# Kernel tuning notes

Measured on AMD Instinct MI355X. Metric: run time of the kernel, lower is better.

Reference implementation:

```python
import jax, jax.numpy as jnp
import numpy as np

T = 2048
HIDDEN = 4096
H = 32
HKV = 8
D = 128
THETA = 10000.0


def setup_inputs() -> dict:
    key = jax.random.key(0)
    k1, k2, k3, k4, k5 = jax.random.split(key, 5)
    s = 0.02
    return {
        "x": jax.random.normal(k1, (T, 2 * HIDDEN), dtype=jnp.float32),
        "positions": jnp.arange(T, dtype=jnp.int32),
        "Wq": jax.random.normal(k2, (H * D, 2 * HIDDEN), dtype=jnp.float32) * s,
        "Wk": jax.random.normal(k3, (HKV * D, 2 * HIDDEN), dtype=jnp.float32) * s,
        "Wv": jax.random.normal(k4, (HKV * D, 2 * HIDDEN), dtype=jnp.float32) * s,
        "Wo": jax.random.normal(k5, (HIDDEN, H * D), dtype=jnp.float32) * s,
    }


def _rope_cos_sin(positions):
    # NeoX-style: cos_sin_cache[pos] = [cos(freqs), sin(freqs)], freqs over head_dim/2
    inv_freq = 1.0 / (THETA ** (jnp.arange(0, D, 2, dtype=jnp.float32) / D))
    freqs = positions.astype(jnp.float32)[:, None] * inv_freq  # [T, D/2]
    return jnp.cos(freqs)[:, None, :], jnp.sin(freqs)[:, None, :]  # broadcast over heads


def _apply_rope(t, cos, sin):
    half = D // 2
    t1, t2 = t[..., :half], t[..., half:]
    return jnp.concatenate([t1 * cos - t2 * sin, t2 * cos + t1 * sin], axis=-1)


def reference(x, positions, Wq, Wk, Wv, Wo):
    n = x.shape[0]
    q = (x @ Wq.T).reshape(n, H, D)
    k = (x @ Wk.T).reshape(n, HKV, D)
    v = (x @ Wv.T).reshape(n, HKV, D)
    cos, sin = _rope_cos_sin(positions)
    q = _apply_rope(q, cos, sin)
    k = _apply_rope(k, cos, sin)
    # cache starts empty -> k_full/v_full are just k/v; prefill (n>1) -> causal
    G = H // HKV  # GQA group size; avoid materializing repeated K/V
    qg = q.reshape(n, HKV, G, D)
    scale = D ** -0.5
    scores = jnp.einsum("tkgd,skd->kgts", qg, k) * scale  # [HKV, G, T, T]
    causal = jnp.arange(n)[:, None] >= jnp.arange(n)[None, :]
    scores = jnp.where(causal, scores, jnp.finfo(scores.dtype).min)
    p = jax.nn.softmax(scores, axis=-1)
    o = jnp.einsum("kgts,skd->tkgd", p, v).reshape(n, H * D)
    return o @ Wo.T
```

## Files before the change

### kernel.cpp

```cpp
#include <hip/hip_runtime.h>
#include <hip/hip_bf16.h>
#include <math.h>

typedef unsigned short u16;
typedef u16 u16x8 __attribute__((ext_vector_type(8)));
typedef __bf16 bf16x8 __attribute__((ext_vector_type(8)));
typedef float f32x4 __attribute__((ext_vector_type(4)));

#define T_SEQ 2048
#define IN_DIM 8192
#define QKV_COLS 6144
#define O_COLS 4096

__device__ __forceinline__ u16 f2bf(float f){
  unsigned u = __builtin_bit_cast(unsigned, f);
  u += 0x7fffu + ((u >> 16) & 1u);
  return (u16)(u >> 16);
}
__device__ __forceinline__ float bf2f(u16 h){
  unsigned u = ((unsigned)h) << 16;
  return __builtin_bit_cast(float, u);
}
__device__ __forceinline__ void gload16(const void* g, void* l){
  __builtin_amdgcn_global_load_lds((const __attribute__((address_space(1))) unsigned*)g,
                                   (__attribute__((address_space(3))) unsigned*)l, 16, 0, 0);
}
__device__ __forceinline__ void storeC(float* p, float v){ *p = v; }
__device__ __forceinline__ void storeC(u16* p, float v){ *p = f2bf(v); }

__global__ void cvt_all(const float* __restrict__ x, const float* __restrict__ wq,
                        const float* __restrict__ wk, const float* __restrict__ wv,
                        const float* __restrict__ wo,
                        u16* __restrict__ xb, u16* __restrict__ wb, u16* __restrict__ wob){
  const int NX  = T_SEQ*IN_DIM/4;
  const int NQ  = 4096*IN_DIM/4;
  const int NKV = 1024*IN_DIM/4;
  const int NO  = 4096*4096/4;
  const int TOT = NX + NQ + 2*NKV + NO;
  int stride = gridDim.x * blockDim.x;
  for (int i = blockIdx.x*blockDim.x + threadIdx.x; i < TOT; i += stride){
    const float4* s; ushort4* d; int j = i;
    if (j < NX){ s = (const float4*)x; d = (ushort4*)xb; }
    else { j -= NX;
      if (j < NQ){ s = (const float4*)wq; d = (ushort4*)wb; }
      else { j -= NQ;
        if (j < NKV){ s = (const float4*)wk; d = (ushort4*)(wb + (size_t)4096*IN_DIM); }
        else { j -= NKV;
          if (j < NKV){ s = (const float4*)wv; d = (ushort4*)(wb + (size_t)5120*IN_DIM); }
          else { j -= NKV; s = (const float4*)wo; d = (ushort4*)wob; } } } }
    float4 v = s[j];
    ushort4 o; o.x = f2bf(v.x); o.y = f2bf(v.y); o.z = f2bf(v.z); o.w = f2bf(v.w);
    d[j] = o;
  }
}

__global__ void rope_scale_kernel(u16* __restrict__ qkv, const int* __restrict__ pos){
  __shared__ float cs[64], sn[64];
  int t = blockIdx.x;
  int p = pos[t];
  if (threadIdx.x < 64){
    int i = threadIdx.x;
    double e = (double)(2*i) / 128.0;
    float invf = (float)pow(10000.0, -e);
    float ang = (float)p * invf;
    cs[i] = cosf(ang);
    sn[i] = sinf(ang);
  }
  __syncthreads();
  u16* row = qkv + (size_t)t * QKV_COLS;
  const float qscale = 0.08838834764831845f;
  for (int idx = threadIdx.x; idx < 40*64; idx += blockDim.x){
    int head = idx >> 6, i = idx & 63;
    int base = (head < 32) ? head*128 : 4096 + (head-32)*128;
    float sc = (head < 32) ? qscale : 1.0f;
    float t1 = bf2f(row[base + i]);
    float t2 = bf2f(row[base + i + 64]);
    row[base + i]      = f2bf((t1*cs[i] - t2*sn[i]) * sc);
    row[base + i + 64] = f2bf((t2*cs[i] + t1*sn[i]) * sc);
  }
}

template<typename OutT, int NFRAG>
__global__ __launch_bounds__(512,2) void gemm_pipe(const u16* __restrict__ A, const u16* __restrict__ B,
                                                   OutT* __restrict__ C, int K, int ldc, int ntile_n){
  __shared__ __attribute__((aligned(16))) u16 Asm[4*8192];
  __shared__ __attribute__((aligned(16))) u16 Bsm[4*NFRAG*2048];
  const int tid = threadIdx.x;
  const int w = tid >> 6, l = tid & 63;
  const int wm = w >> 2, wn = w & 3;
  const int lr = l & 15, lg = l >> 4;
  const int id = blockIdx.x;
  const int m0 = (id & 7) * 256;
  const int n0 = (id >> 3) * (NFRAG*64);
  const int BBUF = NFRAG*4096;

  const int srow  = tid >> 2;
  const int sslot = ((tid & 3) - ((tid >> 3) & 3)) & 3;
  const u16* Ag  = A + (size_t)(m0 + srow) * K + sslot * 8;
  const u16* Bg  = B + (size_t)(n0 + srow) * K + sslot * 8;
  const u16* Bg2 = B + (size_t)(n0 + 128 + srow) * K + sslot * 8;
  char* AsB = (char*)Asm;
  char* BsB = (char*)Bsm;
  const int sdst = w * 1024;

  int aoff[8], boff[NFRAG];
  #pragma unroll
  for (int i = 0; i < 8; ++i){
    int ra = wm*128 + i*16 + lr;
    aoff[i] = ra*64 + (((lg + (ra>>1)) & 3) << 4);
  }
  #pragma unroll
  for (int i = 0; i < NFRAG; ++i){
    int rb = wn*(NFRAG*16) + i*16 + lr;
    boff[i] = rb*64 + (((lg + (rb>>1)) & 3) << 4);
  }

  f32x4 acc[8][NFRAG];
  #pragma unroll
  for (int m = 0; m < 8; ++m)
    #pragma unroll
    for (int n = 0; n < NFRAG; ++n)
      acc[m][n] = (f32x4){0.f,0.f,0.f,0.f};

  const int NT = K >> 5;

  #define STAGE_TILE(tt) do { \
    const int nb_ = ((tt) & 3); \
    gload16(Ag + (tt)*32,                 AsB + nb_*16384 +        sdst); \
    gload16(Ag + (size_t)128*K + (tt)*32, AsB + nb_*16384 + 8192 + sdst); \
    gload16(Bg + (tt)*32,                 BsB + nb_*BBUF +         sdst); \
    if (NFRAG == 3 && tid < 256) \
      gload16(Bg2 + (tt)*32,              BsB + nb_*BBUF + 8192 +  sdst); \
  } while(0)

  STAGE_TILE(0);
  STAGE_TILE(1);

  for (int t = 0; t < NT; ++t){
    const int ab = (t & 3) * 16384;
    const int bb = (t & 3) * BBUF;
    if (t == NT-1){
      asm volatile("s_waitcnt vmcnt(0)" ::: "memory");
    } else if (NFRAG == 3){
      if (w < 4) asm volatile("s_waitcnt vmcnt(4)" ::: "memory");
      else       asm volatile("s_waitcnt vmcnt(3)" ::: "memory");
    } else {
      asm volatile("s_waitcnt vmcnt(3)" ::: "memory");
    }
    __builtin_amdgcn_s_barrier();
    __builtin_amdgcn_sched_barrier(0);

    bf16x8 bfr[NFRAG], afr[8];
    #pragma unroll
    for (int n = 0; n < NFRAG; ++n) bfr[n] = *(const bf16x8*)(BsB + bb + boff[n]);
    #pragma unroll
    for (int i = 0; i < 8; ++i)     afr[i] = *(const bf16x8*)(AsB + ab + aoff[i]);

    if (t + 2 < NT) STAGE_TILE(t+2);

    __builtin_amdgcn_s_setprio(1);
    #pragma unroll
    for (int i = 0; i < 8; ++i)
      #pragma unroll
      for (int n = 0; n < NFRAG; ++n)
        acc[i][n] = __builtin_amdgcn_mfma_f32_16x16x32_bf16(afr[i], bfr[n], acc[i][n], 0, 0, 0);
    __builtin_amdgcn_s_setprio(0);
  }
  #undef STAGE_TILE

  #pragma unroll
  for (int m = 0; m < 8; ++m)
    #pragma unroll
    for (int n = 0; n < NFRAG; ++n)
      #pragma unroll
      for (int r = 0; r < 4; ++r){
        int row = m0 + wm*128 + m*16 + lg*4 + r;
        int col = n0 + wn*(NFRAG*16) + n*16 + lr;
        storeC(&C[(size_t)row*ldc + col], acc[m][n][r]);
      }
}

__global__ __launch_bounds__(256) void attn_kernel(const u16* __restrict__ qkv, u16* __restrict__ ob){
  __shared__ __attribute__((aligned(16))) u16 Ksm[32*128];
  __shared__ __attribute__((aligned(16))) u16 Vt[128*40];
  __shared__ __attribute__((aligned(16))) u16 Psm[4][32*40];
  const int tid = threadIdx.x, l = tid & 63, w = tid >> 6;
  const int lr = l & 15, lg = l >> 4;
  const int qb = (gridDim.x - 1) - blockIdx.x;
  const int kv = blockIdx.y;
  const int h = kv*4 + w;
  const int q0 = qb * 32;

  bf16x8 aq[2][4];
  #pragma unroll
  for (int mm = 0; mm < 2; ++mm)
    #pragma unroll
    for (int kk = 0; kk < 4; ++kk)
      aq[mm][kk] = *(const bf16x8*)(qkv + (size_t)(q0 + mm*16 + lr)*QKV_COLS + h*128 + kk*32 + lg*8);

  f32x4 oacc[2][8] = {};
  float mrun[2][4], lrun[2][4];
  #pragma unroll
  for (int mm=0;mm<2;mm++)
    #pragma unroll
    for (int r=0;r<4;r++){ mrun[mm][r] = -1e30f; lrun[mm][r] = 0.f; }

  const int cbv = ((tid & 15) << 4) | (tid >> 4);
  for (int kt = 0; kt <= qb; ++kt){
    const int s0 = kt * 32;
    #pragma unroll
    for (int i = 0; i < 2; ++i){
      int c = tid + i*256, s = c >> 4, dq = c & 15;
      u16x8 kvv = *(const u16x8*)(qkv + (size_t)(s0+s)*QKV_COLS + 4096 + kv*128 + dq*8);
      int lin = (s << 8) + (dq << 4); lin ^= (s & 7) << 4;
      *(u16x8*)((char*)Ksm + lin) = kvv;
    }
    #pragma unroll
    for (int i = 0; i < 2; ++i){
      int c = cbv + i*256, s = c >> 4, dq = c & 15;
      u16x8 vv = *(const u16x8*)(qkv + (size_t)(s0+s)*QKV_COLS + 5120 + kv*128 + dq*8);
      #pragma unroll
      for (int j = 0; j < 8; ++j) Vt[(dq*8+j)*40 + s] = vv[j];
    }
    __syncthreads();

    f32x4 sa[2][2] = {};
    #pragma unroll
    for (int kk = 0; kk < 4; ++kk){
      bf16x8 bk[2];
      #pragma unroll
      for (int nn = 0; nn < 2; ++nn){
        int srow = nn*16 + lr;
        int lin = (srow << 8) + (kk << 6) + (lg << 4); lin ^= (srow & 7) << 4;
        bk[nn] = *(const bf16x8*)((char*)Ksm + lin);
      }
      #pragma unroll
      for (int mm = 0; mm < 2; ++mm)
        #pragma unroll
        for (int nn = 0; nn < 2; ++nn)
          sa[mm][nn] = __builtin_amdgcn_mfma_f32_16x16x32_bf16(aq[mm][kk], bk[nn], sa[mm][nn], 0,0,0);
    }

    if (kt == qb){
      #pragma unroll
      for (int mm=0;mm<2;mm++)
        #pragma unroll
        for (int nn=0;nn<2;nn++)
          #pragma unroll
          for (int r=0;r<4;r++){
            int qrel = mm*16 + lg*4 + r, srel = nn*16 + lr;
            if (srel > qrel) sa[mm][nn][r] = -1e30f;
          }
    }

    float alph[2][4];
    #pragma unroll
    for (int mm=0;mm<2;mm++)
      #pragma unroll
      for (int r=0;r<4;r++){
        float v = fmaxf(sa[mm][0][r], sa[mm][1][r]);
        v = fmaxf(v, __shfl_xor(v, 1));
        v = fmaxf(v, __shfl_xor(v, 2));
        v = fmaxf(v, __shfl_xor(v, 4));
        v = fmaxf(v, __shfl_xor(v, 8));
        float mn = fmaxf(mrun[mm][r], v);
        float al = __expf(mrun[mm][r] - mn);
        float p0 = __expf(sa[mm][0][r] - mn);
        float p1 = __expf(sa[mm][1][r] - mn);
        sa[mm][0][r] = p0; sa[mm][1][r] = p1;
        float rs = p0 + p1;
        rs += __shfl_xor(rs, 1);
        rs += __shfl_xor(rs, 2);
        rs += __shfl_xor(rs, 4);
        rs += __shfl_xor(rs, 8);
        lrun[mm][r] = lrun[mm][r]*al + rs;
        mrun[mm][r] = mn;
        alph[mm][r] = al;
      }
    #pragma unroll
    for (int mm=0;mm<2;mm++)
      #pragma unroll
      for (int df=0;df<8;df++)
        #pragma unroll
        for (int r=0;r<4;r++)
          oacc[mm][df][r] *= alph[mm][r];

    #pragma unroll
    for (int mm=0;mm<2;mm++)
      #pragma unroll
      for (int nn=0;nn<2;nn++)
        #pragma unroll
        for (int r=0;r<4;r++)
          Psm[w][(mm*16 + lg*4 + r)*40 + nn*16 + lr] = f2bf(sa[mm][nn][r]);

    bf16x8 ap[2];
    #pragma unroll
    for (int mm=0;mm<2;mm++)
      ap[mm] = *(const bf16x8*)(&Psm[w][(mm*16 + lr)*40 + lg*8]);
    #pragma unroll
    for (int df=0;df<8;df++){
      bf16x8 bv = *(const bf16x8*)(&Vt[(df*16 + lr)*40 + lg*8]);
      #pragma unroll
      for (int mm=0;mm<2;mm++)
        oacc[mm][df] = __builtin_amdgcn_mfma_f32_16x16x32_bf16(ap[mm], bv, oacc[mm][df], 0,0,0);
    }
    __syncthreads();
  }

  #pragma unroll
  for (int mm=0;mm<2;mm++)
    #pragma unroll
    for (int df=0;df<8;df++)
      #pragma unroll
      for (int r=0;r<4;r++){
        float val = oacc[mm][df][r] / lrun[mm][r];
        int t = q0 + mm*16 + lg*4 + r;
        int col = h*128 + df*16 + lr;
        ob[(size_t)t*O_COLS + col] = f2bf(val);
      }
}

extern "C" void kernel_launch(void* const* d_in, const int* in_sizes, int n_in,
                              void* d_out, int out_size, void* d_ws, size_t ws_size,
                              hipStream_t stream){
  const float* x  = (const float*)d_in[0];
  const int*   pos= (const int*)d_in[1];
  const float* Wq = (const float*)d_in[2];
  const float* Wk = (const float*)d_in[3];
  const float* Wv = (const float*)d_in[4];
  const float* Wo = (const float*)d_in[5];
  float* out = (float*)d_out;

  char* ws = (char*)d_ws;
  u16* xb   = (u16*)(ws);
  u16* wb   = (u16*)(ws + 33554432);
  u16* wob  = (u16*)(ws + 134217728);
  u16* qkv  = (u16*)(ws + 167772160);
  u16* obuf = (u16*)(ws + 192937984);

  cvt_all<<<2048, 256, 0, stream>>>(x, Wq, Wk, Wv, Wo, xb, wb, wob);

  gemm_pipe<u16,3><<<256, 512, 0, stream>>>(xb, wb, qkv, IN_DIM, QKV_COLS, 32);
  rope_scale_kernel<<<T_SEQ, 256, 0, stream>>>(qkv, pos);
  attn_kernel<<<dim3(64,8), 256, 0, stream>>>(qkv, obuf);
  gemm_pipe<float,2><<<256, 512, 0, stream>>>(obuf, wob, out, O_COLS, O_COLS, 32);
}
```

Measured before the change: 853.3 us.

## Pre-transpose V globally and double-buffer K/V via async LDS loads in attention

Adds a separate kernel that writes V transposed into a workspace buffer, so the attention kernel no longer does per-element scalar transposes into shared memory each tile. The attention kernel now uses 64-key tiles, issues direct global-to-LDS loads for K (double buffered) and V, and uses waitcnt plus barriers so the next tiles load while the current tile computes. It also raises occupancy hints and sets wave priority around the MFMA blocks. The cost is an extra kernel launch and an extra pass over V in global memory, plus more shared memory per block.

After: 782.5 us. 8.3% less time.

```diff
diff --git a/kernel.cpp b/kernel.cpp
--- a/kernel.cpp
+++ b/kernel.cpp
@@ -80,6 +80,29 @@
   }
 }
 
+__global__ void transpose_v(const u16* __restrict__ qkv, u16* __restrict__ vtg){
+  __shared__ u16 tl[128][72];
+  const int head = blockIdx.y;
+  const int st = blockIdx.x;
+  const int tid = threadIdx.x;
+  #pragma unroll
+  for (int i = 0; i < 4; ++i){
+    int c = tid + i*256, s = c >> 4, dq = c & 15;
+    u16x8 v = *(const u16x8*)(qkv + (size_t)(st*64+s)*QKV_COLS + 5120 + head*128 + dq*8);
+    #pragma unroll
+    for (int j = 0; j < 8; ++j) tl[dq*8+j][s] = v[j];
+  }
+  __syncthreads();
+  #pragma unroll
+  for (int i = 0; i < 4; ++i){
+    int c = tid + i*256, d = c >> 3, sq = c & 7;
+    u16x8 v;
+    #pragma unroll
+    for (int j = 0; j < 8; ++j) v[j] = tl[d][sq*8+j];
+    *(u16x8*)(vtg + (size_t)head*262144 + (size_t)d*2048 + st*64 + sq*8) = v;
+  }
+}
+
 template<typename OutT, int NFRAG>
 __global__ __launch_bounds__(512,2) void gemm_pipe(const u16* __restrict__ A, const u16* __restrict__ B,
                                                    OutT* __restrict__ C, int K, int ldc, int ntile_n){
@@ -180,16 +203,18 @@
       }
 }
 
-__global__ __launch_bounds__(256) void attn_kernel(const u16* __restrict__ qkv, u16* __restrict__ ob){
-  __shared__ __attribute__((aligned(16))) u16 Ksm[32*128];
-  __shared__ __attribute__((aligned(16))) u16 Vt[128*40];
-  __shared__ __attribute__((aligned(16))) u16 Psm[4][32*40];
+__global__ __launch_bounds__(256,2) void attn2(const u16* __restrict__ qkv, const u16* __restrict__ vtg,
+                                               u16* __restrict__ ob){
+  __shared__ __attribute__((aligned(16))) u16 Ksm[2*64*128];
+  __shared__ __attribute__((aligned(16))) u16 Vsm[128*64];
+  __shared__ __attribute__((aligned(16))) u16 Psm[4][32*72];
   const int tid = threadIdx.x, l = tid & 63, w = tid >> 6;
   const int lr = l & 15, lg = l >> 4;
-  const int qb = (gridDim.x - 1) - blockIdx.x;
+  const int qb = 63 - (int)blockIdx.x;
   const int kv = blockIdx.y;
   const int h = kv*4 + w;
   const int q0 = qb * 32;
+  const int lastkt = (qb*32 + 31) >> 6;
 
   bf16x8 aq[2][4];
   #pragma unroll
@@ -198,77 +223,92 @@
     for (int kk = 0; kk < 4; ++kk)
       aq[mm][kk] = *(const bf16x8*)(qkv + (size_t)(q0 + mm*16 + lr)*QKV_COLS + h*128 + kk*32 + lg*8);
 
+  const u16* Ksrc[4]; const u16* Vsrc[4];
+  #pragma unroll
+  for (int i = 0; i < 4; ++i){
+    int c = (i*4 + w)*64 + l;
+    int s = c >> 4, cp = c & 15;
+    Ksrc[i] = qkv + (size_t)s*QKV_COLS + 4096 + kv*128 + ((cp ^ (s & 7)) * 8);
+    int d = c >> 3, cp2 = c & 7;
+    Vsrc[i] = vtg + (size_t)kv*262144 + (size_t)d*2048 + ((cp2 ^ (d & 7)) * 8);
+  }
+  char* KsB = (char*)Ksm;
+  char* VsB = (char*)Vsm;
+
+  #define STAGE_K(kt) do { const int bo_ = ((kt)&1)*16384; \
+    _Pragma("unroll") for (int i_ = 0; i_ < 4; ++i_) \
+      gload16(Ksrc[i_] + (size_t)(kt)*64*QKV_COLS, KsB + bo_ + (i_*4+w)*1024); } while(0)
+  #define STAGE_V(kt) do { \
+    _Pragma("unroll") for (int i_ = 0; i_ < 4; ++i_) \
+      gload16(Vsrc[i_] + (kt)*64, VsB + (i_*4+w)*1024); } while(0)
+
+  STAGE_K(0);
+  STAGE_V(0);
+  if (lastkt >= 1) STAGE_K(1);
+
   f32x4 oacc[2][8] = {};
   float mrun[2][4], lrun[2][4];
   #pragma unroll
-  for (int mm=0;mm<2;mm++)
-    #pragma unroll
-    for (int r=0;r<4;r++){ mrun[mm][r] = -1e30f; lrun[mm][r] = 0.f; }
-
-  const int cbv = ((tid & 15) << 4) | (tid >> 4);
-  for (int kt = 0; kt <= qb; ++kt){
-    const int s0 = kt * 32;
-    #pragma unroll
-    for (int i = 0; i < 2; ++i){
-      int c = tid + i*256, s = c >> 4, dq = c & 15;
-      u16x8 kvv = *(const u16x8*)(qkv + (size_t)(s0+s)*QKV_COLS + 4096 + kv*128 + dq*8);
-      int lin = (s << 8) + (dq << 4); lin ^= (s & 7) << 4;
-      *(u16x8*)((char*)Ksm + lin) = kvv;
-    }
-    #pragma unroll
-    for (int i = 0; i < 2; ++i){
-      int c = cbv + i*256, s = c >> 4, dq = c & 15;
-      u16x8 vv = *(const u16x8*)(qkv + (size_t)(s0+s)*QKV_COLS + 5120 + kv*128 + dq*8);
-      #pragma unroll
-      for (int j = 0; j < 8; ++j) Vt[(dq*8+j)*40 + s] = vv[j];
-    }
-    __syncthreads();
-
-    f32x4 sa[2][2] = {};
+  for (int mm = 0; mm < 2; ++mm)
+    #pragma unroll
+    for (int r = 0; r < 4; ++r){ mrun[mm][r] = -1e30f; lrun[mm][r] = 0.f; }
+
+  for (int kt = 0; kt <= lastkt; ++kt){
+    if (kt < lastkt) asm volatile("s_waitcnt vmcnt(8)" ::: "memory");
+    else             asm volatile("s_waitcnt vmcnt(4)" ::: "memory");
+    __builtin_amdgcn_s_barrier();
+    const int kb = (kt & 1) * 16384;
+
+    f32x4 sa[2][4] = {};
+    __builtin_amdgcn_s_setprio(1);
     #pragma unroll
     for (int kk = 0; kk < 4; ++kk){
-      bf16x8 bk[2];
-      #pragma unroll
-      for (int nn = 0; nn < 2; ++nn){
-        int srow = nn*16 + lr;
-        int lin = (srow << 8) + (kk << 6) + (lg << 4); lin ^= (srow & 7) << 4;
-        bk[nn] = *(const bf16x8*)((char*)Ksm + lin);
+      bf16x8 bk[4];
+      #pragma unroll
+      for (int nn = 0; nn < 4; ++nn){
+        int row = nn*16 + lr;
+        bk[nn] = *(const bf16x8*)(KsB + kb + row*256 + (((kk*4 + lg) ^ (row & 7)) << 4));
       }
       #pragma unroll
       for (int mm = 0; mm < 2; ++mm)
         #pragma unroll
-        for (int nn = 0; nn < 2; ++nn)
+        for (int nn = 0; nn < 4; ++nn)
           sa[mm][nn] = __builtin_amdgcn_mfma_f32_16x16x32_bf16(aq[mm][kk], bk[nn], sa[mm][nn], 0,0,0);
     }
-
-    if (kt == qb){
-      #pragma unroll
-      for (int mm=0;mm<2;mm++)
-        #pragma unroll
-        for (int nn=0;nn<2;nn++)
+    __builtin_amdgcn_s_setprio(0);
+
+    if (kt == lastkt){
+      #pragma unroll
+      for (int mm = 0; mm < 2; ++mm)
+        #pragma unroll
+        for (int nn = 0; nn < 4; ++nn)
           #pragma unroll
-          for (int r=0;r<4;r++){
-            int qrel = mm*16 + lg*4 + r, srel = nn*16 + lr;
+          for (int r = 0; r < 4; ++r){
+            int srel = kt*64 + nn*16 + lr;
+            int qrel = q0 + mm*16 + lg*4 + r;
             if (srel > qrel) sa[mm][nn][r] = -1e30f;
           }
     }
 
     float alph[2][4];
     #pragma unroll
-    for (int mm=0;mm<2;mm++)
-      #pragma unroll
-      for (int r=0;r<4;r++){
-        float v = fmaxf(sa[mm][0][r], sa[mm][1][r]);
+    for (int mm = 0; mm < 2; ++mm)
+      #pragma unroll
+      for (int r = 0; r < 4; ++r){
+        float v = fmaxf(fmaxf(sa[mm][0][r], sa[mm][1][r]), fmaxf(sa[mm][2][r], sa[mm][3][r]));
         v = fmaxf(v, __shfl_xor(v, 1));
         v = fmaxf(v, __shfl_xor(v, 2));
         v = fmaxf(v, __shfl_xor(v, 4));
         v = fmaxf(v, __shfl_xor(v, 8));
         float mn = fmaxf(mrun[mm][r], v);
         float al = __expf(mrun[mm][r] - mn);
-        float p0 = __expf(sa[mm][0][r] - mn);
-        float p1 = __expf(sa[mm][1][r] - mn);
-        sa[mm][0][r] = p0; sa[mm][1][r] = p1;
-        float rs = p0 + p1;
+        float rs = 0.f;
+        #pragma unroll
+        for (int nn = 0; nn < 4; ++nn){
+          float p = __expf(sa[mm][nn][r] - mn);
+          sa[mm][nn][r] = p;
+          rs += p;
+        }
         rs += __shfl_xor(rs, 1);
         rs += __shfl_xor(rs, 2);
         rs += __shfl_xor(rs, 4);
@@ -278,41 +318,63 @@
         alph[mm][r] = al;
       }
     #pragma unroll
-    for (int mm=0;mm<2;mm++)
-      #pragma unroll
-      for (int df=0;df<8;df++)
-        #pragma unroll
-        for (int r=0;r<4;r++)
+    for (int mm = 0; mm < 2; ++mm)
+      #pragma unroll
+      for (int df = 0; df < 8; ++df)
+        #pragma unroll
+        for (int r = 0; r < 4; ++r)
           oacc[mm][df][r] *= alph[mm][r];
 
-    #pragma unroll
-    for (int mm=0;mm<2;mm++)
-      #pragma unroll
-      for (int nn=0;nn<2;nn++)
-        #pragma unroll
-        for (int r=0;r<4;r++)
-          Psm[w][(mm*16 + lg*4 + r)*40 + nn*16 + lr] = f2bf(sa[mm][nn][r]);
-
-    bf16x8 ap[2];
-    #pragma unroll
-    for (int mm=0;mm<2;mm++)
-      ap[mm] = *(const bf16x8*)(&Psm[w][(mm*16 + lr)*40 + lg*8]);
-    #pragma unroll
-    for (int df=0;df<8;df++){
-      bf16x8 bv = *(const bf16x8*)(&Vt[(df*16 + lr)*40 + lg*8]);
-      #pragma unroll
-      for (int mm=0;mm<2;mm++)
-        oacc[mm][df] = __builtin_amdgcn_mfma_f32_16x16x32_bf16(ap[mm], bv, oacc[mm][df], 0,0,0);
+    if (kt < lastkt) asm volatile("s_waitcnt vmcnt(4)" ::: "memory");
+    else             asm volatile("s_waitcnt vmcnt(0)" ::: "memory");
+    __builtin_amdgcn_s_barrier();
+
+    #pragma unroll
+    for (int mm = 0; mm < 2; ++mm)
+      #pragma unroll
+      for (int nn = 0; nn < 4; ++nn)
+        #pragma unroll
+        for (int r = 0; r < 4; ++r)
+          Psm[w][(mm*16 + lg*4 + r)*72 + nn*16 + lr] = f2bf(sa[mm][nn][r]);
+
+    bf16x8 ap[2][2];
+    #pragma unroll
+    for (int mm = 0; mm < 2; ++mm)
+      #pragma unroll
+      for (int ks = 0; ks < 2; ++ks)
+        ap[mm][ks] = *(const bf16x8*)(&Psm[w][(mm*16 + lr)*72 + ks*32 + lg*8]);
+
+    __builtin_amdgcn_s_setprio(1);
+    #pragma unroll
+    for (int df = 0; df < 8; ++df){
+      bf16x8 bv[2];
+      #pragma unroll
+      for (int ks = 0; ks < 2; ++ks){
+        int d = df*16 + lr;
+        bv[ks] = *(const bf16x8*)(VsB + d*128 + (((ks*4 + lg) ^ (d & 7)) << 4));
+      }
+      #pragma unroll
+      for (int mm = 0; mm < 2; ++mm)
+        #pragma unroll
+        for (int ks = 0; ks < 2; ++ks)
+          oacc[mm][df] = __builtin_amdgcn_mfma_f32_16x16x32_bf16(ap[mm][ks], bv[ks], oacc[mm][df], 0,0,0);
     }
-    __syncthreads();
-  }
-
-  #pragma unroll
-  for (int mm=0;mm<2;mm++)
-    #pragma unroll
-    for (int df=0;df<8;df++)
-      #pragma unroll
-      for (int r=0;r<4;r++){
+    __builtin_amdgcn_s_setprio(0);
+
+    asm volatile("" ::: "memory");
+    __builtin_amdgcn_s_barrier();
+    if (kt + 1 <= lastkt) STAGE_V(kt+1);
+    if (kt + 2 <= lastkt) STAGE_K(kt+2);
+  }
+  #undef STAGE_K
+  #undef STAGE_V
+
+  #pragma unroll
+  for (int mm = 0; mm < 2; ++mm)
+    #pragma unroll
+    for (int df = 0; df < 8; ++df)
+      #pragma unroll
+      for (int r = 0; r < 4; ++r){
         float val = oacc[mm][df][r] / lrun[mm][r];
         int t = q0 + mm*16 + lg*4 + r;
         int col = h*128 + df*16 + lr;
@@ -337,11 +399,13 @@
   u16* wob  = (u16*)(ws + 134217728);
   u16* qkv  = (u16*)(ws + 167772160);
   u16* obuf = (u16*)(ws + 192937984);
+  u16* vtg  = (u16*)(ws + 209715200);
 
   cvt_all<<<2048, 256, 0, stream>>>(x, Wq, Wk, Wv, Wo, xb, wb, wob);
 
   gemm_pipe<u16,3><<<256, 512, 0, stream>>>(xb, wb, qkv, IN_DIM, QKV_COLS, 32);
+  transpose_v<<<dim3(32,8), 256, 0, stream>>>(qkv, vtg);
   rope_scale_kernel<<<T_SEQ, 256, 0, stream>>>(qkv, pos);
-  attn_kernel<<<dim3(64,8), 256, 0, stream>>>(qkv, obuf);
+  attn2<<<dim3(64,8), 256, 0, stream>>>(qkv, vtg, obuf);
   gemm_pipe<float,2><<<256, 512, 0, stream>>>(obuf, wob, out, O_COLS, O_COLS, 32);
 }
```
